# Performance work log

Hardware: AMD Instinct MI355X
Metric: run time of the kernel (lower is better)

## Reference

```python
import jax, jax.numpy as jnp
import numpy as np

B, V, T = 256, 128000, 16
TOP_K = 100          # min(100, V - n_targets) == 100 since V >> T
TARGET_MARGIN = 1.0
EPS = 1e-8
NEG = -1e30          # sentinel so masked target slots never enter top-k


def setup_inputs() -> dict:
    key = jax.random.key(0)
    k1, k2 = jax.random.split(key)
    # Non-negative sparse activations (SPLADE-style relu output) in [0,1)
    sparse_rep = jax.random.uniform(k1, (B, V), dtype=jnp.float32)
    # Fixed-length padded target id lists (all rows valid -> n_valid = B)
    target_ids = jax.random.randint(k2, (B, T), 0, V).astype(jnp.int64)
    return {"sparse_rep": sparse_rep, "target_ids": target_ids}


def reference(sparse_rep, target_ids):
    # [B, T] gather of target activations (one batched gather, no per-row loop)
    tgt = jnp.take_along_axis(sparse_rep, target_ids, axis=1)
    # -log(a + eps), per-row mean then batch mean == global mean (fixed T)
    target_loss = -jnp.mean(jnp.log(tgt + EPS))
    # hinge margin on target activations
    margin_loss = jnp.mean(jax.nn.relu(TARGET_MARGIN - tgt))
    # mask out target columns per row, then top-k over remaining vocab
    rows = jnp.arange(sparse_rep.shape[0])[:, None]          # [B, 1]
    masked = sparse_rep.at[rows, target_ids].set(NEG)        # [B, V]
    top_vals = jax.lax.top_k(masked, TOP_K)[0]               # [B, TOP_K]
    negative_loss = jnp.mean(top_vals)
    return (target_loss, margin_loss, negative_loss)
```

## Files before the change

kernel.cpp:

```cpp
#include <hip/hip_runtime.h>
#include <cstddef>
#include <cstdint>

#define B_      256
#define V_      128000
#define T_      16
#define TOPK_   100
#define NF4     (V_ / 4)
#define NHIST   4096
#define SLICES  25
#define F4S     (NF4 / SLICES)
#define ITERS   (F4S / 256)
#define CAP_BLK 128
#define CAP_ROW 4096
#define T0      0.998f


__global__ void zero_kernel(float* o, int* ws_cnt, int* ws_of) {
    int t = threadIdx.x;
    if (t < 3) o[t] = 0.f;
    if (t < B_) { ws_cnt[t] = 0; ws_of[t] = 0; }
}

__global__ __launch_bounds__(256) void collect_kernel(
        const float* __restrict__ sparse,
        const int*   __restrict__ tids,
        float*       __restrict__ ws_cand,
        int*         __restrict__ ws_cnt,
        int*         __restrict__ ws_of) {
    __shared__ int   s_ids[T_];
    __shared__ float s_buf[CAP_BLK];
    __shared__ int   s_n;
    __shared__ int   s_gbase;

    const int blk = blockIdx.x;
    const int row = blk / SLICES;
    const int sl  = blk - row * SLICES;
    const int tid = threadIdx.x;

    if (tid < T_) s_ids[tid] = tids[row * T_ + tid];
    if (tid == 0) s_n = 0;
    __syncthreads();

    const float4* __restrict__ rp4 = (const float4*)(sparse + (size_t)row * V_);
    const int base = sl * F4S + tid;

    float4 v[ITERS];
    #pragma unroll
    for (int u = 0; u < ITERS; ++u)
        v[u] = rp4[base + u * 256];

    #pragma unroll
    for (int u = 0; u < ITERS; ++u) {
        const int col = (base + u * 256) << 2;
        float xs[4] = {v[u].x, v[u].y, v[u].z, v[u].w};
        #pragma unroll
        for (int c = 0; c < 4; ++c) {
            float x = xs[c];
            if (x >= T0) {
                int cc = col + c;
                bool is_t = false;
                #pragma unroll
                for (int j = 0; j < T_; ++j) is_t |= (cc == s_ids[j]);
                if (!is_t) {
                    int k = atomicAdd(&s_n, 1);
                    if (k < CAP_BLK) s_buf[k] = x;
                }
            }
        }
    }
    __syncthreads();

    int n = min(s_n, CAP_BLK);
    if (tid == 0) {
        s_gbase = atomicAdd(ws_cnt + row, n);
        if (s_n > CAP_BLK) atomicExch(ws_of + row, 1);
    }
    __syncthreads();
    int gbase = s_gbase;
    float* __restrict__ cand = ws_cand + (size_t)row * CAP_ROW;
    for (int i = tid; i < n; i += 256) {
        int idx = gbase + i;
        if (idx < CAP_ROW) cand[idx] = s_buf[i];
        else if (tid == 0) atomicExch(ws_of + row, 1);
    }
}

__global__ __launch_bounds__(256) void reduce_kernel(
        const float* __restrict__ sparse,
        const int*   __restrict__ tids,
        const float* __restrict__ ws_cand,
        const int*   __restrict__ ws_cnt,
        const int*   __restrict__ ws_of,
        float*       __restrict__ out) {
    __shared__ float s_cand[CAP_ROW];
    __shared__ int   s_ids[T_];
    __shared__ int   s_cnt;
    __shared__ int   s_bstar;
    __shared__ float s_red[4];

    const int row = blockIdx.x;
    const int tid = threadIdx.x;
    const float* __restrict__ rp = sparse + (size_t)row * V_;

    if (tid < T_) s_ids[tid] = tids[row * T_ + tid];
    __syncthreads();

    if (tid < T_) {
        float x  = rp[s_ids[tid]];
        float tl = -logf(x + 1e-8f);
        float ml = fmaxf(1.0f - x, 0.0f);
        #pragma unroll
        for (int off = 8; off > 0; off >>= 1) {
            tl += __shfl_down(tl, off);
            ml += __shfl_down(ml, off);
        }
        if (tid == 0) {
            atomicAdd(out + 0, tl * (1.0f / (B_ * T_)));
            atomicAdd(out + 1, ml * (1.0f / (B_ * T_)));
        }
    }

    int cnt = ws_cnt[row];
    bool bad = (cnt < TOPK_) || (cnt > CAP_ROW) || (ws_of[row] != 0);

    if (!bad) {
        const float* cand = ws_cand + (size_t)row * CAP_ROW;
        for (int i = tid; i < cnt; i += 256) s_cand[i] = cand[i];
        __syncthreads();
    } else {
        unsigned* s_hist = (unsigned*)s_cand;
        for (int i = tid; i < NHIST; i += 256) s_hist[i] = 0u;
        if (tid == 0) s_cnt = 0;
        __syncthreads();
        const float4* rp4 = (const float4*)rp;
        for (int i = tid; i < NF4; i += 256) {
            float4 v = rp4[i];
            float xs[4] = {v.x, v.y, v.z, v.w};
            #pragma unroll
            for (int c = 0; c < 4; ++c) {
                int b = (int)(xs[c] * (float)NHIST);
                b = min(max(b, 0), NHIST - 1);
                atomicAdd(&s_hist[b], 1u);
            }
        }
        __syncthreads();
        if (tid == 0) {
            for (int j = 0; j < T_; ++j) {
                int id = s_ids[j];
                bool dup = false;
                for (int q = 0; q < j; ++q) dup = dup || (s_ids[q] == id);
                if (!dup) {
                    int b = (int)(rp[id] * (float)NHIST);
                    b = min(max(b, 0), NHIST - 1);
                    s_hist[b]--;
                }
            }
            int acc = 0, b = NHIST - 1;
            for (; b >= 0; --b) {
                acc += (int)s_hist[b];
                if (acc >= TOPK_) break;
            }
            s_bstar = max(b, 0);
        }
        __syncthreads();
        int bstar = s_bstar;
        for (int i = tid; i < NF4; i += 256) {
            float4 v = rp4[i];
            int col = i << 2;
            float xs[4] = {v.x, v.y, v.z, v.w};
            #pragma unroll
            for (int c = 0; c < 4; ++c) {
                float x = xs[c];
                int b = (int)(x * (float)NHIST);
                b = min(max(b, 0), NHIST - 1);
                if (b >= bstar) {
                    int cc = col + c;
                    bool is_t = false;
                    #pragma unroll
                    for (int j = 0; j < T_; ++j) is_t |= (cc == s_ids[j]);
                    if (!is_t) {
                        int k = atomicAdd(&s_cnt, 1);
                        if (k < CAP_ROW) s_cand[k] = x;
                    }
                }
            }
        }
        __syncthreads();
        cnt = min(s_cnt, CAP_ROW);
    }

    float sum = 0.f;
    for (int i = tid; i < cnt; i += 256) {
        float x = s_cand[i];
        int rank = 0;
        for (int j = 0; j < cnt; ++j) {
            float y = s_cand[j];
            rank += (y > x) ? 1 : ((y == x && j < i) ? 1 : 0);
        }
        if (rank < TOPK_) sum += x;
    }

    #pragma unroll
    for (int off = 32; off > 0; off >>= 1) sum += __shfl_down(sum, off);
    if ((tid & 63) == 0) s_red[tid >> 6] = sum;
    __syncthreads();
    if (tid == 0) {
        float tot = s_red[0] + s_red[1] + s_red[2] + s_red[3];
        atomicAdd(out + 2, tot * (1.0f / (B_ * TOPK_)));
    }
}

extern "C" void kernel_launch(void* const* d_in, const int* in_sizes, int n_in,
                              void* d_out, int out_size, void* d_ws, size_t ws_size,
                              hipStream_t stream) {
    const float* sparse = (const float*)d_in[0];
    const int*   tids   = (const int*)d_in[1];
    float*       out    = (float*)d_out;
    int*         ws_cnt  = (int*)d_ws;
    int*         ws_of   = (int*)((char*)d_ws + 1024);
    float*       ws_cand = (float*)((char*)d_ws + 4096);

    zero_kernel<<<1, 256, 0, stream>>>(out, ws_cnt, ws_of);
    collect_kernel<<<B_ * SLICES, 256, 0, stream>>>(sparse, tids, ws_cand, ws_cnt, ws_of);
    reduce_kernel<<<B_, 256, 0, stream>>>(sparse, tids, ws_cand, ws_cnt, ws_of, out);
}
```

Measured before the change: 213.2 us.

## Drop zero kernel, use per-block candidate slots, add float4 max prefilter

Removes the separate zero kernel: output zeroing moves into block 0 of collect, and global per-row atomics are replaced by fixed per-block candidate slots with counts that reduce_kernel prefix-sums. Adds a cheap max-of-four prefilter so most float4 groups skip the per-element threshold and target checks. Each block now holds at most 32 candidates, so a slice with more than 32 above-threshold values sends its row to the slow histogram fallback. Zeroing out in block 0 relies on collect finishing before reduce_kernel's atomic adds, which stream order provides.

Measured after the change: 212.8 us. About the same (-0.2%).

```diff
diff --git a/kernel.cpp b/kernel.cpp
--- a/kernel.cpp
+++ b/kernel.cpp
@@ -11,33 +11,28 @@
 #define SLICES  25
 #define F4S     (NF4 / SLICES)
 #define ITERS   (F4S / 256)
-#define CAP_BLK 128
-#define CAP_ROW 4096
+#define CAP_BLK 32
+#define NBLK    (B_ * SLICES)
 #define T0      0.998f
 
-
-__global__ void zero_kernel(float* o, int* ws_cnt, int* ws_of) {
-    int t = threadIdx.x;
-    if (t < 3) o[t] = 0.f;
-    if (t < B_) { ws_cnt[t] = 0; ws_of[t] = 0; }
-}
 
 __global__ __launch_bounds__(256) void collect_kernel(
         const float* __restrict__ sparse,
         const int*   __restrict__ tids,
         float*       __restrict__ ws_cand,
-        int*         __restrict__ ws_cnt,
-        int*         __restrict__ ws_of) {
+        int*         __restrict__ ws_bcnt,
+        float*       __restrict__ out) {
     __shared__ int   s_ids[T_];
     __shared__ float s_buf[CAP_BLK];
     __shared__ int   s_n;
-    __shared__ int   s_gbase;
 
     const int blk = blockIdx.x;
     const int row = blk / SLICES;
     const int sl  = blk - row * SLICES;
     const int tid = threadIdx.x;
 
+    if (blk == 0 && tid < 3) out[tid] = 0.f;
+
     if (tid < T_) s_ids[tid] = tids[row * T_ + tid];
     if (tid == 0) s_n = 0;
     __syncthreads();
@@ -52,49 +47,45 @@
 
     #pragma unroll
     for (int u = 0; u < ITERS; ++u) {
-        const int col = (base + u * 256) << 2;
-        float xs[4] = {v[u].x, v[u].y, v[u].z, v[u].w};
-        #pragma unroll
-        for (int c = 0; c < 4; ++c) {
-            float x = xs[c];
-            if (x >= T0) {
-                int cc = col + c;
-                bool is_t = false;
-                #pragma unroll
-                for (int j = 0; j < T_; ++j) is_t |= (cc == s_ids[j]);
-                if (!is_t) {
-                    int k = atomicAdd(&s_n, 1);
-                    if (k < CAP_BLK) s_buf[k] = x;
+        float m = fmaxf(fmaxf(v[u].x, v[u].y), fmaxf(v[u].z, v[u].w));
+        if (m >= T0) {
+            const int col = (base + u * 256) << 2;
+            float xs[4] = {v[u].x, v[u].y, v[u].z, v[u].w};
+            #pragma unroll
+            for (int c = 0; c < 4; ++c) {
+                float x = xs[c];
+                if (x >= T0) {
+                    int cc = col + c;
+                    bool is_t = false;
+                    #pragma unroll
+                    for (int j = 0; j < T_; ++j) is_t |= (cc == s_ids[j]);
+                    if (!is_t) {
+                        int k = atomicAdd(&s_n, 1);
+                        if (k < CAP_BLK) s_buf[k] = x;
+                    }
                 }
             }
         }
     }
     __syncthreads();
 
-    int n = min(s_n, CAP_BLK);
-    if (tid == 0) {
-        s_gbase = atomicAdd(ws_cnt + row, n);
-        if (s_n > CAP_BLK) atomicExch(ws_of + row, 1);
-    }
-    __syncthreads();
-    int gbase = s_gbase;
-    float* __restrict__ cand = ws_cand + (size_t)row * CAP_ROW;
-    for (int i = tid; i < n; i += 256) {
-        int idx = gbase + i;
-        if (idx < CAP_ROW) cand[idx] = s_buf[i];
-        else if (tid == 0) atomicExch(ws_of + row, 1);
-    }
+    int n = s_n;
+    if (tid == 0) ws_bcnt[blk] = n;
+    if (tid < n && tid < CAP_BLK)
+        ws_cand[(size_t)blk * CAP_BLK + tid] = s_buf[tid];
 }
 
 __global__ __launch_bounds__(256) void reduce_kernel(
         const float* __restrict__ sparse,
         const int*   __restrict__ tids,
         const float* __restrict__ ws_cand,
-        const int*   __restrict__ ws_cnt,
-        const int*   __restrict__ ws_of,
+        const int*   __restrict__ ws_bcnt,
         float*       __restrict__ out) {
-    __shared__ float s_cand[CAP_ROW];
+    __shared__ float s_cand[NHIST];
     __shared__ int   s_ids[T_];
+    __shared__ int   s_cnts[SLICES];
+    __shared__ int   s_off[SLICES + 1];
+    __shared__ int   s_bad;
     __shared__ int   s_cnt;
     __shared__ int   s_bstar;
     __shared__ float s_red[4];
@@ -104,6 +95,7 @@
     const float* __restrict__ rp = sparse + (size_t)row * V_;
 
     if (tid < T_) s_ids[tid] = tids[row * T_ + tid];
+    if (tid < SLICES) s_cnts[tid] = ws_bcnt[row * SLICES + tid];
     __syncthreads();
 
     if (tid < T_) {
@@ -121,12 +113,31 @@
         }
     }
 
-    int cnt = ws_cnt[row];
-    bool bad = (cnt < TOPK_) || (cnt > CAP_ROW) || (ws_of[row] != 0);
-
-    if (!bad) {
-        const float* cand = ws_cand + (size_t)row * CAP_ROW;
-        for (int i = tid; i < cnt; i += 256) s_cand[i] = cand[i];
+    if (tid == 0) {
+        int acc = 0, bad = 0;
+        #pragma unroll
+        for (int s = 0; s < SLICES; ++s) {
+            int c = s_cnts[s];
+            if (c > CAP_BLK) bad = 1;
+            s_off[s] = acc;
+            acc += min(c, CAP_BLK);
+        }
+        s_off[SLICES] = acc;
+        if (acc < TOPK_) bad = 1;
+        s_bad = bad;
+    }
+    __syncthreads();
+
+    int cnt;
+    if (!s_bad) {
+        cnt = s_off[SLICES];
+        const int wave = tid >> 6, lane = tid & 63;
+        for (int s = wave; s < SLICES; s += 4) {
+            int c = min(s_cnts[s], CAP_BLK);
+            if (lane < c)
+                s_cand[s_off[s] + lane] =
+                    ws_cand[(size_t)(row * SLICES + s) * CAP_BLK + lane];
+        }
         __syncthreads();
     } else {
         unsigned* s_hist = (unsigned*)s_cand;
@@ -181,13 +192,13 @@
                     for (int j = 0; j < T_; ++j) is_t |= (cc == s_ids[j]);
                     if (!is_t) {
                         int k = atomicAdd(&s_cnt, 1);
-                        if (k < CAP_ROW) s_cand[k] = x;
+                        if (k < NHIST) s_cand[k] = x;
                     }
                 }
             }
         }
         __syncthreads();
-        cnt = min(s_cnt, CAP_ROW);
+        cnt = min(s_cnt, NHIST);
     }
 
     float sum = 0.f;
@@ -214,14 +225,12 @@
 extern "C" void kernel_launch(void* const* d_in, const int* in_sizes, int n_in,
                               void* d_out, int out_size, void* d_ws, size_t ws_size,
                               hipStream_t stream) {
-    const float* sparse = (const float*)d_in[0];
-    const int*   tids   = (const int*)d_in[1];
-    float*       out    = (float*)d_out;
-    int*         ws_cnt  = (int*)d_ws;
-    int*         ws_of   = (int*)((char*)d_ws + 1024);
-    float*       ws_cand = (float*)((char*)d_ws + 4096);
-
-    zero_kernel<<<1, 256, 0, stream>>>(out, ws_cnt, ws_of);
-    collect_kernel<<<B_ * SLICES, 256, 0, stream>>>(sparse, tids, ws_cand, ws_cnt, ws_of);
-    reduce_kernel<<<B_, 256, 0, stream>>>(sparse, tids, ws_cand, ws_cnt, ws_of, out);
+    const float* sparse  = (const float*)d_in[0];
+    const int*   tids    = (const int*)d_in[1];
+    float*       out     = (float*)d_out;
+    int*         ws_bcnt = (int*)d_ws;
+    float*       ws_cand = (float*)((char*)d_ws + 32768);
+
+    collect_kernel<<<NBLK, 256, 0, stream>>>(sparse, tids, ws_cand, ws_bcnt, out);
+    reduce_kernel<<<B_, 256, 0, stream>>>(sparse, tids, ws_cand, ws_bcnt, out);
 }
```
